# Kernel tuning notes

Hardware: AMD Instinct MI355X
Metric: run time of the kernel (lower is better)

The kernel has to match this reference:

```python
import jax, jax.numpy as jnp
import numpy as np

D_MODEL = 1024
N_HEADS = 16
D_K = D_MODEL // N_HEADS
B, S = 8, 1024
EPS = 1e-8


def setup_inputs() -> dict:
    key = jax.random.key(0)
    ks = jax.random.split(key, 6)
    scale = 1.0 / np.sqrt(D_MODEL)
    return {
        "Q_in": jax.random.normal(ks[0], (B, S, D_MODEL), jnp.float32),
        "mask": jax.random.randint(ks[1], (B, 1, S, S), 0, 2, jnp.int32),
        "Wq": jax.random.normal(ks[2], (D_MODEL, D_MODEL), jnp.float32) * scale,
        "bq": jnp.zeros((D_MODEL,), jnp.float32),
        "Wk": jax.random.normal(ks[3], (D_MODEL, D_MODEL), jnp.float32) * scale,
        "bk": jnp.zeros((D_MODEL,), jnp.float32),
        "Wv": jax.random.normal(ks[4], (D_MODEL, D_MODEL), jnp.float32) * scale,
        "bv": jnp.zeros((D_MODEL,), jnp.float32),
        "Wo": jax.random.normal(ks[5], (D_MODEL, D_MODEL), jnp.float32) * scale,
        "bo": jnp.zeros((D_MODEL,), jnp.float32),
    }


def reference(Q_in, mask, Wq, bq, Wk, bk, Wv, bv, Wo, bo):
    # QKV projections: [B,S,D] -> [B,H,S,d_k]
    def split_heads(x):
        return x.reshape(B, S, N_HEADS, D_K).transpose(0, 2, 1, 3)

    Q = split_heads(Q_in @ Wq + bq)
    K = split_heads(Q_in @ Wk + bk)
    V = split_heads(Q_in @ Wv + bv)

    # scaled scores [B,H,S,S], standard softmax
    scores = jnp.einsum("bhqd,bhkd->bhqk", Q, K) / jnp.sqrt(
        jnp.asarray(D_K, jnp.float32))
    scores = jax.nn.softmax(scores, axis=-1)
    # non-standard: multiplicative mask AFTER softmax, then row renorm
    scores = scores * mask.astype(scores.dtype)
    attn = scores / (jnp.sum(scores, axis=-1, keepdims=True) + EPS)

    context = jnp.einsum("bhqk,bhkd->bhqd", attn, V)
    context = context.transpose(0, 2, 1, 3).reshape(B, S, D_MODEL)
    return context @ Wo + bo
```

## Files before the change

kernel.cpp:

```cpp
#include <hip/hip_runtime.h>
#include <hip/hip_bf16.h>
#include <stdint.h>

typedef __attribute__((ext_vector_type(4))) float f32x4;
typedef __attribute__((ext_vector_type(8))) __bf16 bf16x8;
typedef unsigned short u16;
typedef unsigned int u32;
typedef unsigned long long u64;

#define NH 16
#define DKK 64

__device__ __forceinline__ u16 f2bf(float f) {
    u32 u = __builtin_bit_cast(u32, f);
    u32 r = (u + 0x7fffu + ((u >> 16) & 1u)) >> 16;
    return (u16)r;
}

__device__ __forceinline__ u16 cvt_bf(float f) {
    __hip_bfloat16 h = __float2bfloat16(f);
    return *reinterpret_cast<u16*>(&h);
}

__device__ __forceinline__ void gload16(const void* g, void* l) {
    __builtin_amdgcn_global_load_lds((const __attribute__((address_space(1))) void*)g,
                                     (__attribute__((address_space(3))) void*)l, 16, 0, 0);
}

__global__ __launch_bounds__(256) void k_convert_x(const float* __restrict__ x,
                                                   u16* __restrict__ xb) {
    int i = blockIdx.x * 256 + threadIdx.x;
    const float4* p = (const float4*)x + (size_t)i * 2;
    float4 a = p[0], b = p[1];
    union { u16 h[8]; uint4 q; } o;
    o.h[0] = f2bf(a.x); o.h[1] = f2bf(a.y); o.h[2] = f2bf(a.z); o.h[3] = f2bf(a.w);
    o.h[4] = f2bf(b.x); o.h[5] = f2bf(b.y); o.h[6] = f2bf(b.z); o.h[7] = f2bf(b.w);
    ((uint4*)xb)[i] = o.q;
}

__global__ __launch_bounds__(256) void k_convert_w(const float* __restrict__ wq,
                                                   const float* __restrict__ wk,
                                                   const float* __restrict__ wv,
                                                   const float* __restrict__ wo,
                                                   u16* __restrict__ wt) {
    int z = blockIdx.z;
    const float* w = (z == 0) ? wq : (z == 1) ? wk : (z == 2) ? wv : wo;
    __shared__ float t[32][33];
    int tx = threadIdx.x & 31, ty = threadIdx.x >> 5;
    int n0 = blockIdx.x * 32, k0 = blockIdx.y * 32;
    for (int rr = 0; rr < 4; ++rr)
        t[ty + rr * 8][tx] = w[(size_t)(k0 + ty + rr * 8) * 1024 + n0 + tx];
    __syncthreads();
    for (int rr = 0; rr < 4; ++rr) {
        int n = n0 + ty + rr * 8;
        wt[((size_t)z * 1024 + n) * 1024 + k0 + tx] = f2bf(t[tx][ty + rr * 8]);
    }
}

__global__ __launch_bounds__(256) void k_maskpack(const int* __restrict__ mask,
                                                  u64* __restrict__ mb) {
    int wid = (blockIdx.x * 256 + threadIdx.x) >> 6;
    int lane = threadIdx.x & 63;
    for (int c = wid; c < 8 * 1024 * 16; c += 8192) {
        int m = mask[(size_t)c * 64 + lane];
        u64 bits = __ballot(m != 0);
        if (lane == 0)
            mb[(c & 0xFFFFC000u) | ((c & 15) << 10) | ((c >> 4) & 1023)] = bits;
    }
}

template <int MODE>
__global__ __launch_bounds__(256) void k_gemm(const u16* __restrict__ A,
                                              const u16* __restrict__ Bt,
                                              const float* __restrict__ b0,
                                              const float* __restrict__ b1,
                                              const float* __restrict__ b2,
                                              u16* __restrict__ q_out,
                                              u16* __restrict__ k_out,
                                              u16* __restrict__ v_out,
                                              float* __restrict__ out) {
    __shared__ u16 As[128 * 32];
    __shared__ u16 Bs[128 * 32];
    int tid = threadIdx.x;
    int wv = tid >> 6, lane = tid & 63;
    int r = lane & 15, g = lane >> 4;
    int wr = wv >> 1, wc = wv & 1;
    int m0 = blockIdx.x * 128, n0 = blockIdx.y * 128;
    f32x4 acc[4][4] = {};
    for (int kt = 0; kt < 1024; kt += 32) {
        __syncthreads();
        for (int i = 0; i < 2; ++i) {
            int e = i * 256 + tid;
            int row = e >> 2;
            int cs = ((e & 3) ^ ((row >> 1) & 3)) * 8;
            const u16* ga = A + (size_t)(m0 + row) * 1024 + kt + cs;
            const u16* gb = Bt + (size_t)(n0 + row) * 1024 + kt + cs;
            gload16(ga, As + (size_t)(i * 256 + wv * 64) * 8);
            gload16(gb, Bs + (size_t)(i * 256 + wv * 64) * 8);
        }
        __syncthreads();
        bf16x8 aF[4], bF[4];
#pragma unroll
        for (int m = 0; m < 4; ++m) {
            int ro = wr * 64 + m * 16 + r;
            aF[m] = *(const bf16x8*)&As[ro * 32 + ((g ^ ((ro >> 1) & 3)) << 3)];
        }
#pragma unroll
        for (int n = 0; n < 4; ++n) {
            int ro = wc * 64 + n * 16 + r;
            bF[n] = *(const bf16x8*)&Bs[ro * 32 + ((g ^ ((ro >> 1) & 3)) << 3)];
        }
#pragma unroll
        for (int m = 0; m < 4; ++m)
#pragma unroll
            for (int n = 0; n < 4; ++n)
                acc[m][n] = __builtin_amdgcn_mfma_f32_16x16x32_bf16(aF[m], bF[n], acc[m][n], 0, 0, 0);
    }
    for (int m = 0; m < 4; ++m) {
        int rowb = m0 + wr * 64 + m * 16 + 4 * g;
        for (int n = 0; n < 4; ++n) {
            int col = n0 + wc * 64 + n * 16 + r;
            if (MODE == 0) {
                int w = col >> 10, cn = col & 1023;
                const float* bp = (w == 0) ? b0 : (w == 1) ? b1 : b2;
                u16* dst = (w == 0) ? q_out : (w == 1) ? k_out : v_out;
                float sc = (w == 0) ? 0.125f : 1.0f;
                int h = cn >> 6, d = cn & 63;
                float bias = bp[cn];
                for (int i = 0; i < 4; ++i) {
                    int row = rowb + i;
                    int b = row >> 10, s = row & 1023;
                    float v = (acc[m][n][i] + bias) * sc;
                    dst[((size_t)(b * NH + h) * 1024 + s) * 64 + d] = f2bf(v);
                }
            } else {
                float bias = b0[col];
                for (int i = 0; i < 4; ++i) {
                    int row = rowb + i;
                    out[(size_t)row * 1024 + col] = acc[m][n][i] + bias;
                }
            }
        }
    }
}

__global__ __launch_bounds__(256) void k_transpose_v(const u16* __restrict__ vb,
                                                     u16* __restrict__ vt) {
    __shared__ u16 t[64][72];
    int bh = blockIdx.y, s0 = blockIdx.x * 64;
    int tid = threadIdx.x;
    for (int i = 0; i < 2; ++i) {
        int e = i * 256 + tid;
        int row = e >> 3, ch = (e & 7) * 8;
        uint4 v = *(const uint4*)(vb + ((size_t)bh * 1024 + s0 + row) * 64 + ch);
        *(uint4*)&t[row][ch] = v;
    }
    __syncthreads();
    for (int i = 0; i < 2; ++i) {
        int e = i * 256 + tid;
        int d = e >> 3, ch = (e & 7) * 8;
        union { u16 h[8]; uint4 q; } o;
        for (int j = 0; j < 8; ++j) o.h[j] = t[ch + j][d];
        *(uint4*)(vt + ((size_t)bh * 64 + d) * 1024 + s0 + ch) = o.q;
    }
}

__global__ __launch_bounds__(256, 3) void k_attn(const u16* __restrict__ qb,
                                                 const u16* __restrict__ kb,
                                                 const u16* __restrict__ vt,
                                                 const u64* __restrict__ mbits,
                                                 u16* __restrict__ ctx) {
    __shared__ u16 Kd[2][64 * 64];
    __shared__ u16 Vd[2][64 * 64];
    int tid = threadIdx.x, wv = tid >> 6, lane = tid & 63;
    int r = lane & 15, g = lane >> 4;
    int q0 = blockIdx.x * 128, bh = blockIdx.y;
    int b = bh >> 4, h = bh & 15;

    bf16x8 aq[2][2];
    for (int qg = 0; qg < 2; ++qg) {
        const u16* qp = qb + ((size_t)bh * 1024 + q0 + wv * 32 + qg * 16 + r) * 64 + g * 8;
        aq[qg][0] = *(const bf16x8*)qp;
        aq[qg][1] = *(const bf16x8*)(qp + 32);
    }

    f32x4 of[2][4] = {};
    f32x4 zacc[2] = {};
    const bf16x8 vone = {(__bf16)1.f, (__bf16)1.f, (__bf16)1.f, (__bf16)1.f,
                         (__bf16)1.f, (__bf16)1.f, (__bf16)1.f, (__bf16)1.f};

    const u64* mrow = mbits + ((size_t)b * 16) * 1024 + q0 + wv * 32 + r;
    u64 mbc[2] = {mrow[0], mrow[16]};

    for (int i2 = 0; i2 < 2; ++i2) {
        int e = i2 * 256 + tid;
        int s = e >> 3, c = e & 7;
        int cs = (c ^ (s & 7)) * 8;
        int kr = (s & 0x20) | ((s & 0x0C) << 1) | ((s & 0x10) >> 2) | (s & 3);
        gload16(kb + ((size_t)bh * 1024 + kr) * 64 + cs, Kd[0] + (size_t)e * 8);
        gload16(vt + ((size_t)bh * 64 + s) * 1024 + cs, Vd[0] + (size_t)e * 8);
    }
    __syncthreads();

    for (int t = 0; t < 16; ++t) {
        int cur = t & 1;
        u64 mbn0 = 0, mbn1 = 0;
        if (t < 15) {
            int ktn = (t + 1) * 64;
            for (int i2 = 0; i2 < 2; ++i2) {
                int e = i2 * 256 + tid;
                int s = e >> 3, c = e & 7;
                int cs = (c ^ (s & 7)) * 8;
                int kr = (s & 0x20) | ((s & 0x0C) << 1) | ((s & 0x10) >> 2) | (s & 3);
                gload16(kb + ((size_t)bh * 1024 + ktn + kr) * 64 + cs, Kd[cur ^ 1] + (size_t)e * 8);
                gload16(vt + ((size_t)bh * 64 + s) * 1024 + ktn + cs, Vd[cur ^ 1] + (size_t)e * 8);
            }
            mbn0 = mrow[(size_t)(t + 1) * 1024];
            mbn1 = mrow[(size_t)(t + 1) * 1024 + 16];
        }
        const u16* K = Kd[cur];
        const u16* V = Vd[cur];

        bf16x8 bk0[4], bk1[4];
#pragma unroll
        for (int nf = 0; nf < 4; ++nf) {
            int rowk = (nf * 16 + r) * 64;
            bk0[nf] = *(const bf16x8*)&K[rowk + ((g ^ (r & 7)) << 3)];
            bk1[nf] = *(const bf16x8*)&K[rowk + (((g + 4) ^ (r & 7)) << 3)];
        }

        bf16x8 pfr[2][2];
#pragma unroll
        for (int qg = 0; qg < 2; ++qg) {
            f32x4 sf[4];
#pragma unroll
            for (int nf = 0; nf < 4; ++nf) {
                f32x4 z = {0.f, 0.f, 0.f, 0.f};
                z = __builtin_amdgcn_mfma_f32_16x16x32_bf16(bk0[nf], aq[qg][0], z, 0, 0, 0);
                sf[nf] = __builtin_amdgcn_mfma_f32_16x16x32_bf16(bk1[nf], aq[qg][1], z, 0, 0, 0);
            }
            u64 m64 = mbc[qg] >> (g * 8);
            u32 mlo = (u32)m64, mhi = (u32)(m64 >> 32);
            u32 pw[8];
#pragma unroll
            for (int nf = 0; nf < 4; ++nf) {
                u32 nib = ((nf & 2) ? mhi : mlo) >> ((nf & 1) * 4);
                u32 pm0 = ((nib & 1) ? 0xFFFFu : 0u) | ((nib & 2) ? 0xFFFF0000u : 0u);
                u32 pm1 = ((nib & 4) ? 0xFFFFu : 0u) | ((nib & 8) ? 0xFFFF0000u : 0u);
                float e0 = __expf(sf[nf][0]), e1 = __expf(sf[nf][1]);
                float e2 = __expf(sf[nf][2]), e3 = __expf(sf[nf][3]);
                pw[2 * nf]     = (((u32)cvt_bf(e0)) | ((u32)cvt_bf(e1) << 16)) & pm0;
                pw[2 * nf + 1] = (((u32)cvt_bf(e2)) | ((u32)cvt_bf(e3) << 16)) & pm1;
            }
            union { u32 w[4]; bf16x8 v; } f0, f1;
            f0.w[0] = pw[0]; f0.w[1] = pw[1]; f0.w[2] = pw[2]; f0.w[3] = pw[3];
            f1.w[0] = pw[4]; f1.w[1] = pw[5]; f1.w[2] = pw[6]; f1.w[3] = pw[7];
            pfr[qg][0] = f0.v;
            pfr[qg][1] = f1.v;
            zacc[qg] = __builtin_amdgcn_mfma_f32_16x16x32_bf16(vone, pfr[qg][0], zacc[qg], 0, 0, 0);
            zacc[qg] = __builtin_amdgcn_mfma_f32_16x16x32_bf16(vone, pfr[qg][1], zacc[qg], 0, 0, 0);
        }
#pragma unroll
        for (int ks = 0; ks < 2; ++ks) {
#pragma unroll
            for (int nf = 0; nf < 4; ++nf) {
                bf16x8 av = *(const bf16x8*)&V[(nf * 16 + r) * 64 + (((ks * 4 + g) ^ (r & 7)) << 3)];
                of[0][nf] = __builtin_amdgcn_mfma_f32_16x16x32_bf16(av, pfr[0][ks], of[0][nf], 0, 0, 0);
                of[1][nf] = __builtin_amdgcn_mfma_f32_16x16x32_bf16(av, pfr[1][ks], of[1][nf], 0, 0, 0);
            }
        }
        mbc[0] = mbn0;
        mbc[1] = mbn1;
        __syncthreads();
    }

    for (int qg = 0; qg < 2; ++qg) {
        float inv = 1.0f / zacc[qg][0];
        int qrow = q0 + wv * 32 + qg * 16 + r;
        u16* crow = ctx + ((size_t)(b * 1024 + qrow)) * 1024 + h * 64;
#pragma unroll
        for (int nf = 0; nf < 4; ++nf) {
            u32 w0 = ((u32)cvt_bf(of[qg][nf][0] * inv)) | ((u32)cvt_bf(of[qg][nf][1] * inv) << 16);
            u32 w1 = ((u32)cvt_bf(of[qg][nf][2] * inv)) | ((u32)cvt_bf(of[qg][nf][3] * inv) << 16);
            *(u32*)(crow + nf * 16 + g * 4) = w0;
            *(u32*)(crow + nf * 16 + g * 4 + 2) = w1;
        }
    }
}

extern "C" void kernel_launch(void* const* d_in, const int* in_sizes, int n_in,
                              void* d_out, int out_size, void* d_ws, size_t ws_size,
                              hipStream_t stream) {
    const float* Q_in = (const float*)d_in[0];
    const int*   mask = (const int*)d_in[1];
    const float* Wq = (const float*)d_in[2];
    const float* bq = (const float*)d_in[3];
    const float* Wk = (const float*)d_in[4];
    const float* bk = (const float*)d_in[5];
    const float* Wv = (const float*)d_in[6];
    const float* bv = (const float*)d_in[7];
    const float* Wo = (const float*)d_in[8];
    const float* bo = (const float*)d_in[9];

    char* ws = (char*)d_ws;
    u16* Xb = (u16*)(ws);
    u16* Wt = (u16*)(ws + 16777216);
    u16* Qb = (u16*)(ws + 25165824);
    u16* Kb = (u16*)(ws + 41943040);
    u16* Vb = (u16*)(ws + 58720256);
    u16* Vt = (u16*)(ws + 75497472);
    u64* Mb = (u64*)(ws + 92274688);
    u16* Ctx = Vb;

    k_convert_x<<<4096, 256, 0, stream>>>(Q_in, Xb);
    k_convert_w<<<dim3(32, 32, 4), 256, 0, stream>>>(Wq, Wk, Wv, Wo, Wt);
    k_maskpack<<<2048, 256, 0, stream>>>(mask, Mb);
    k_gemm<0><<<dim3(64, 24), 256, 0, stream>>>(Xb, Wt, bq, bk, bv, Qb, Kb, Vb, nullptr);
    k_transpose_v<<<dim3(16, 128), 256, 0, stream>>>(Vb, Vt);
    k_attn<<<dim3(8, 128), 256, 0, stream>>>(Qb, Kb, Vt, Mb, Ctx);
    k_gemm<1><<<dim3(64, 8), 256, 0, stream>>>(Ctx, Wt + (size_t)3 * 1024 * 1024,
                                               bo, nullptr, nullptr,
                                               nullptr, nullptr, nullptr, (float*)d_out);
}
```

Baseline: 176.7 us.

## Fuse prep kernels, use exp2 with folded log2e scale, add MFMA priority hints

```diff
diff --git a/kernel.cpp b/kernel.cpp
--- a/kernel.cpp
+++ b/kernel.cpp
@@ -10,6 +10,7 @@
 
 #define NH 16
 #define DKK 64
+#define QSCALE 0.18033688011112042f
 
 __device__ __forceinline__ u16 f2bf(float f) {
     u32 u = __builtin_bit_cast(u32, f);
@@ -22,50 +23,56 @@
     return *reinterpret_cast<u16*>(&h);
 }
 
+__device__ __forceinline__ float exp2_fast(float x) {
+    return __builtin_amdgcn_exp2f(x);
+}
+
 __device__ __forceinline__ void gload16(const void* g, void* l) {
     __builtin_amdgcn_global_load_lds((const __attribute__((address_space(1))) void*)g,
                                      (__attribute__((address_space(3))) void*)l, 16, 0, 0);
 }
 
-__global__ __launch_bounds__(256) void k_convert_x(const float* __restrict__ x,
-                                                   u16* __restrict__ xb) {
-    int i = blockIdx.x * 256 + threadIdx.x;
-    const float4* p = (const float4*)x + (size_t)i * 2;
-    float4 a = p[0], b = p[1];
-    union { u16 h[8]; uint4 q; } o;
-    o.h[0] = f2bf(a.x); o.h[1] = f2bf(a.y); o.h[2] = f2bf(a.z); o.h[3] = f2bf(a.w);
-    o.h[4] = f2bf(b.x); o.h[5] = f2bf(b.y); o.h[6] = f2bf(b.z); o.h[7] = f2bf(b.w);
-    ((uint4*)xb)[i] = o.q;
-}
-
-__global__ __launch_bounds__(256) void k_convert_w(const float* __restrict__ wq,
-                                                   const float* __restrict__ wk,
-                                                   const float* __restrict__ wv,
-                                                   const float* __restrict__ wo,
-                                                   u16* __restrict__ wt) {
-    int z = blockIdx.z;
-    const float* w = (z == 0) ? wq : (z == 1) ? wk : (z == 2) ? wv : wo;
-    __shared__ float t[32][33];
-    int tx = threadIdx.x & 31, ty = threadIdx.x >> 5;
-    int n0 = blockIdx.x * 32, k0 = blockIdx.y * 32;
-    for (int rr = 0; rr < 4; ++rr)
-        t[ty + rr * 8][tx] = w[(size_t)(k0 + ty + rr * 8) * 1024 + n0 + tx];
-    __syncthreads();
-    for (int rr = 0; rr < 4; ++rr) {
-        int n = n0 + ty + rr * 8;
-        wt[((size_t)z * 1024 + n) * 1024 + k0 + tx] = f2bf(t[tx][ty + rr * 8]);
-    }
-}
-
-__global__ __launch_bounds__(256) void k_maskpack(const int* __restrict__ mask,
-                                                  u64* __restrict__ mb) {
-    int wid = (blockIdx.x * 256 + threadIdx.x) >> 6;
-    int lane = threadIdx.x & 63;
-    for (int c = wid; c < 8 * 1024 * 16; c += 8192) {
-        int m = mask[(size_t)c * 64 + lane];
-        u64 bits = __ballot(m != 0);
-        if (lane == 0)
-            mb[(c & 0xFFFFC000u) | ((c & 15) << 10) | ((c >> 4) & 1023)] = bits;
+__global__ __launch_bounds__(256) void k_prep(const float* __restrict__ x,
+                                              u16* __restrict__ xb,
+                                              const float* __restrict__ wq,
+                                              const float* __restrict__ wk,
+                                              const float* __restrict__ wv,
+                                              const float* __restrict__ wo,
+                                              u16* __restrict__ wt,
+                                              const int* __restrict__ mask,
+                                              u64* __restrict__ mb) {
+    int bx = blockIdx.x;
+    if (bx < 4096) {
+        int i = bx * 256 + threadIdx.x;
+        const float4* p = (const float4*)x + (size_t)i * 2;
+        float4 a = p[0], b = p[1];
+        union { u16 h[8]; uint4 q; } o;
+        o.h[0] = f2bf(a.x); o.h[1] = f2bf(a.y); o.h[2] = f2bf(a.z); o.h[3] = f2bf(a.w);
+        o.h[4] = f2bf(b.x); o.h[5] = f2bf(b.y); o.h[6] = f2bf(b.z); o.h[7] = f2bf(b.w);
+        ((uint4*)xb)[i] = o.q;
+    } else if (bx < 8192) {
+        int idx = bx - 4096;
+        int z = idx >> 10;
+        const float* w = (z == 0) ? wq : (z == 1) ? wk : (z == 2) ? wv : wo;
+        __shared__ float t[32][33];
+        int tx = threadIdx.x & 31, ty = threadIdx.x >> 5;
+        int n0 = (idx & 31) * 32, k0 = ((idx >> 5) & 31) * 32;
+        for (int rr = 0; rr < 4; ++rr)
+            t[ty + rr * 8][tx] = w[(size_t)(k0 + ty + rr * 8) * 1024 + n0 + tx];
+        __syncthreads();
+        for (int rr = 0; rr < 4; ++rr) {
+            int n = n0 + ty + rr * 8;
+            wt[((size_t)z * 1024 + n) * 1024 + k0 + tx] = f2bf(t[tx][ty + rr * 8]);
+        }
+    } else {
+        int wid = ((bx - 8192) * 256 + threadIdx.x) >> 6;
+        int lane = threadIdx.x & 63;
+        for (int c = wid; c < 8 * 1024 * 16; c += 8192) {
+            int m = mask[(size_t)c * 64 + lane];
+            u64 bits = __ballot(m != 0);
+            if (lane == 0)
+                mb[(c & 0xFFFFC000u) | ((c & 15) << 10) | ((c >> 4) & 1023)] = bits;
+        }
     }
 }
 
@@ -124,7 +131,7 @@
                 int w = col >> 10, cn = col & 1023;
                 const float* bp = (w == 0) ? b0 : (w == 1) ? b1 : b2;
                 u16* dst = (w == 0) ? q_out : (w == 1) ? k_out : v_out;
-                float sc = (w == 0) ? 0.125f : 1.0f;
+                float sc = (w == 0) ? QSCALE : 1.0f;
                 int h = cn >> 6, d = cn & 63;
                 float bias = bp[cn];
                 for (int i = 0; i < 4; ++i) {
@@ -178,6 +185,7 @@
     int b = bh >> 4, h = bh & 15;
 
     bf16x8 aq[2][2];
+#pragma unroll
     for (int qg = 0; qg < 2; ++qg) {
         const u16* qp = qb + ((size_t)bh * 1024 + q0 + wv * 32 + qg * 16 + r) * 64 + g * 8;
         aq[qg][0] = *(const bf16x8*)qp;
@@ -233,12 +241,14 @@
 #pragma unroll
         for (int qg = 0; qg < 2; ++qg) {
             f32x4 sf[4];
+            __builtin_amdgcn_s_setprio(1);
 #pragma unroll
             for (int nf = 0; nf < 4; ++nf) {
                 f32x4 z = {0.f, 0.f, 0.f, 0.f};
                 z = __builtin_amdgcn_mfma_f32_16x16x32_bf16(bk0[nf], aq[qg][0], z, 0, 0, 0);
                 sf[nf] = __builtin_amdgcn_mfma_f32_16x16x32_bf16(bk1[nf], aq[qg][1], z, 0, 0, 0);
             }
+            __builtin_amdgcn_s_setprio(0);
             u64 m64 = mbc[qg] >> (g * 8);
             u32 mlo = (u32)m64, mhi = (u32)(m64 >> 32);
             u32 pw[8];
@@ -247,8 +257,8 @@
                 u32 nib = ((nf & 2) ? mhi : mlo) >> ((nf & 1) * 4);
                 u32 pm0 = ((nib & 1) ? 0xFFFFu : 0u) | ((nib & 2) ? 0xFFFF0000u : 0u);
                 u32 pm1 = ((nib & 4) ? 0xFFFFu : 0u) | ((nib & 8) ? 0xFFFF0000u : 0u);
-                float e0 = __expf(sf[nf][0]), e1 = __expf(sf[nf][1]);
-                float e2 = __expf(sf[nf][2]), e3 = __expf(sf[nf][3]);
+                float e0 = exp2_fast(sf[nf][0]), e1 = exp2_fast(sf[nf][1]);
+                float e2 = exp2_fast(sf[nf][2]), e3 = exp2_fast(sf[nf][3]);
                 pw[2 * nf]     = (((u32)cvt_bf(e0)) | ((u32)cvt_bf(e1) << 16)) & pm0;
                 pw[2 * nf + 1] = (((u32)cvt_bf(e2)) | ((u32)cvt_bf(e3) << 16)) & pm1;
             }
@@ -257,9 +267,12 @@
             f1.w[0] = pw[4]; f1.w[1] = pw[5]; f1.w[2] = pw[6]; f1.w[3] = pw[7];
             pfr[qg][0] = f0.v;
             pfr[qg][1] = f1.v;
+            __builtin_amdgcn_s_setprio(1);
             zacc[qg] = __builtin_amdgcn_mfma_f32_16x16x32_bf16(vone, pfr[qg][0], zacc[qg], 0, 0, 0);
             zacc[qg] = __builtin_amdgcn_mfma_f32_16x16x32_bf16(vone, pfr[qg][1], zacc[qg], 0, 0, 0);
-        }
+            __builtin_amdgcn_s_setprio(0);
+        }
+        __builtin_amdgcn_s_setprio(1);
 #pragma unroll
         for (int ks = 0; ks < 2; ++ks) {
 #pragma unroll
@@ -269,11 +282,13 @@
                 of[1][nf] = __builtin_amdgcn_mfma_f32_16x16x32_bf16(av, pfr[1][ks], of[1][nf], 0, 0, 0);
             }
         }
+        __builtin_amdgcn_s_setprio(0);
         mbc[0] = mbn0;
         mbc[1] = mbn1;
         __syncthreads();
     }
 
+#pragma unroll
     for (int qg = 0; qg < 2; ++qg) {
         float inv = 1.0f / zacc[qg][0];
         int qrow = q0 + wv * 32 + qg * 16 + r;
@@ -312,9 +327,7 @@
     u64* Mb = (u64*)(ws + 92274688);
     u16* Ctx = Vb;
 
-    k_convert_x<<<4096, 256, 0, stream>>>(Q_in, Xb);
-    k_convert_w<<<dim3(32, 32, 4), 256, 0, stream>>>(Wq, Wk, Wv, Wo, Wt);
-    k_maskpack<<<2048, 256, 0, stream>>>(mask, Mb);
+    k_prep<<<10240, 256, 0, stream>>>(Q_in, Xb, Wq, Wk, Wv, Wo, Wt, mask, Mb);
     k_gemm<0><<<dim3(64, 24), 256, 0, stream>>>(Xb, Wt, bq, bk, bv, Qb, Kb, Vb, nullptr);
     k_transpose_v<<<dim3(16, 128), 256, 0, stream>>>(Vb, Vt);
     k_attn<<<dim3(8, 128), 256, 0, stream>>>(Qb, Kb, Vt, Mb, Ctx);
```

After: 173.3 us, median of 2. Within noise of the previous version (-1.9%).
